# Optimization experiments

Hardware: AMD Instinct MI355X
Metric: run time of the kernel (lower is better)

## Reference

```python
import jax, jax.numpy as jnp
import numpy as np

IN_DIM, OUT_DIM = 128, 128
NUM, K = 5, 3            # knot intervals, spline order
SIZE = IN_DIM * OUT_DIM
BATCH = 512
NOISE = 0.1


def extend_knots_uniform(grid, k):
    # grid: (s, n_knots). Uniformly extend by k knots on each side.
    if k <= 0:
        return grid
    step = (grid[:, -1:] - grid[:, :1]) / (grid.shape[1] - 1)  # (s,1)
    left = grid[:, :1] - step * jnp.arange(k, 0, -1, dtype=grid.dtype)[None, :]
    right = grid[:, -1:] + step * jnp.arange(1, k + 1, dtype=grid.dtype)[None, :]
    return jnp.concatenate([left, grid, right], axis=1)


def cox_deboor(x, t, k):
    # x: (s, n), t: (s, m) extended knots -> B: (s, m-1-k, n)
    xt = x[:, None, :]                                   # (s,1,n)
    B = ((xt >= t[:, :-1, None]) & (xt < t[:, 1:, None])).astype(x.dtype)  # (s, m-1, n)
    m = t.shape[1]
    for r in range(1, k + 1):
        denom_a = jnp.maximum(t[:, r:m - 1] - t[:, :m - 1 - r], 1e-14)
        alpha = (xt - t[:, :m - 1 - r, None]) / denom_a[:, :, None]
        denom_b = jnp.maximum(t[:, r + 1:m] - t[:, 1:m - r], 1e-14)
        beta = (t[:, r + 1:m, None] - xt) / denom_b[:, :, None]
        B = alpha * B[:, :-1, :] + beta * B[:, 1:, :]    # (s, m-1-r, n)
    return B


def setup_inputs() -> dict:
    key = jax.random.key(0)
    kx, kc = jax.random.split(key)
    x = jax.random.normal(kx, (BATCH, IN_DIM), dtype=jnp.float32)
    knots = jnp.linspace(-1.0, 1.0, NUM + 1, dtype=jnp.float32)
    grid = jnp.tile(knots[None, :], (SIZE, 1))                       # (size, num+1)
    coef = jax.random.normal(kc, (SIZE, NUM + K), dtype=jnp.float32) * NOISE
    scale_base = jnp.ones((SIZE,), dtype=jnp.float32)
    scale_sp = jnp.ones((SIZE,), dtype=jnp.float32)
    mask = jnp.ones((SIZE,), dtype=jnp.float32)
    return {"x": x, "grid": grid, "coef": coef,
            "scale_base": scale_base, "scale_sp": scale_sp, "mask": mask}


def reference(x, grid, coef, scale_base, scale_sp, mask):
    batch = x.shape[0]
    # einsum('ij,k->ikj').reshape(b, size).T : row o*in_dim+i holds x[:, i]
    x_exp = jnp.tile(x, (1, OUT_DIM)).T                  # (size, batch)
    base_act = jax.nn.silu(x_exp)
    t_ext = extend_knots_uniform(grid, K)                # (size, num+1+2k)
    B = cox_deboor(x_exp, t_ext, K)                      # (size, num+k, batch)
    spline_val = jnp.einsum('sbn,sb->sn', B, coef)       # (size, batch)
    out = (scale_base[:, None] * base_act + scale_sp[:, None] * spline_val) * mask[:, None]
    out3 = out.reshape(OUT_DIM, IN_DIM, batch)           # permute(2,0,1).sum(dim=2)
    return out3.sum(axis=1).T                            # (batch, out_dim)
```

## Files before the change

### kernel.cpp

```cpp
#include <hip/hip_runtime.h>
#include <math.h>

constexpr int IN_DIM  = 128;
constexpr int OUT_DIM = 128;
constexpr int BATCH   = 512;
constexpr int TN  = 8;
constexpr int TO  = 32;
constexpr int IC  = 16;
constexpr int NC  = IN_DIM / IC;
constexpr int TOP = TO + 1;

__global__ __launch_bounds__(256, 1) void kan_fused(
    const float* __restrict__ x,
    const float* __restrict__ grid,
    const float* __restrict__ coef,
    const float* __restrict__ scale_base,
    const float* __restrict__ scale_sp,
    const float* __restrict__ mask,
    float* __restrict__ out)
{
    __shared__ float4 Ps[TN * IN_DIM * 2];
    __shared__ float  Pb[IN_DIM * TN];
    __shared__ float4 Cs0[IC * TOP];
    __shared__ float4 Cs1[IC * TOP];
    __shared__ float  Vb [IC * TOP];

    const int t  = threadIdx.x;
    const int b  = blockIdx.x;
    const int o0 = (b & 3) * TO;
    const int n0 = (b >> 2) * TN;

    const float g0 = grid[0];
    const float g5 = grid[5];
    const float h  = (g5 - g0) * 0.2f;
    float tk[12];
    tk[0] = g0 - 3.f * h; tk[1] = g0 - 2.f * h; tk[2] = g0 - h;
    tk[3] = grid[0]; tk[4] = grid[1]; tk[5] = grid[2];
    tk[6] = grid[3]; tk[7] = grid[4]; tk[8] = grid[5];
    tk[9] = g5 + h; tk[10] = g5 + 2.f * h; tk[11] = g5 + 3.f * h;
    const float inv1 = 1.0f / h;
    const float invr[3] = {inv1, inv1 * 0.5f, inv1 * (1.0f / 3.0f)};

    #pragma unroll
    for (int r = 0; r < 4; r++) {
        const int v = r * 256 + t;
        const int n = v >> 7;
        const int i = v & 127;
        const float xv = x[(n0 + n) * IN_DIM + i];
        float B[11];
        #pragma unroll
        for (int j = 0; j < 11; j++)
            B[j] = (xv >= tk[j] && xv < tk[j + 1]) ? 1.0f : 0.0f;
        #pragma unroll
        for (int rr = 1; rr <= 3; rr++) {
            const float iv = invr[rr - 1];
            #pragma unroll
            for (int j = 0; j + rr < 11; j++)
                B[j] = (xv - tk[j]) * iv * B[j] + (tk[j + rr + 1] - xv) * iv * B[j + 1];
        }
        Ps[(n * IN_DIM + i) * 2 + 0] = make_float4(B[0], B[1], B[2], B[3]);
        Ps[(n * IN_DIM + i) * 2 + 1] = make_float4(B[4], B[5], B[6], B[7]);
        Pb[i * TN + n] = xv / (1.0f + __expf(-xv));
    }

    float4 rc[4];
    float  rv[2];

#define LOADREG(cc)                                                          \
    {                                                                        \
        _Pragma("unroll")                                                    \
        for (int r = 0; r < 4; r++) {                                        \
            const int fi = r * 256 + t;                                      \
            const int oo = fi >> 5;                    \
            const int w  = fi & 31;                \
            const int s  = (o0 + oo) * IN_DIM + (cc) * IC + (w >> 1);        \
            float4 cv = ((const float4*)coef)[(size_t)s * 2 + (w & 1)];      \
            const float vv = scale_sp[s] * mask[s];                          \
            cv.x *= vv; cv.y *= vv; cv.z *= vv; cv.w *= vv;                  \
            rc[r] = cv;                                                      \
        }                                                                    \
        _Pragma("unroll")                                                    \
        for (int r = 0; r < 2; r++) {                                        \
            const int v  = r * 256 + t;                                      \
            const int oo = v >> 4;                    \
            const int s  = (o0 + oo) * IN_DIM + (cc) * IC + (v & 15);        \
            rv[r] = scale_base[s] * mask[s];                                 \
        }                                                                    \
    }

#define WRITELDS()                                                           \
    {                                                                        \
        _Pragma("unroll")                                                    \
        for (int r = 0; r < 4; r++) {                                        \
            const int fi = r * 256 + t;                                      \
            const int oo = fi >> 5;                                          \
            const int w  = fi & 31;                                          \
            const int i  = w >> 1;                                           \
            if (w & 1) Cs1[i * TOP + oo] = rc[r];                            \
            else       Cs0[i * TOP + oo] = rc[r];                            \
        }                                                                    \
        _Pragma("unroll")                                                    \
        for (int r = 0; r < 2; r++) {                                        \
            const int v = r * 256 + t;                                       \
            Vb[(v & 15) * TOP + (v >> 4)] = rv[r];                           \
        }                                                                    \
    }

    LOADREG(0);
    WRITELDS();
    __syncthreads();

    const int o = t & 31;
    const int n = t >> 5;
    const float4* __restrict__ psn = &Ps[n * IN_DIM * 2];
    const float*  __restrict__ pbn = &Pb[n];

    float acc = 0.f;
    #pragma unroll 1
    for (int c = 0; c < NC; c++) {
        if (c + 1 < NC) LOADREG(c + 1);
        #pragma unroll
        for (int il = 0; il < IC; il++) {
            const int i = c * IC + il;
            const float4 c0 = Cs0[il * TOP + o];
            const float4 c1 = Cs1[il * TOP + o];
            const float4 a0 = psn[2 * i];
            const float4 a1 = psn[2 * i + 1];
            const float vb  = Vb[il * TOP + o];
            const float pb  = pbn[i * TN];
            acc += c0.x * a0.x + c0.y * a0.y + c0.z * a0.z + c0.w * a0.w
                 + c1.x * a1.x + c1.y * a1.y + c1.z * a1.z + c1.w * a1.w
                 + vb * pb;
        }
        if (c + 1 < NC) {
            __syncthreads();
            WRITELDS();
            __syncthreads();
        }
    }

    out[(size_t)(n0 + n) * OUT_DIM + o0 + o] = acc;
#undef LOADREG
#undef WRITELDS
}

extern "C" void kernel_launch(void* const* d_in, const int* in_sizes, int n_in,
                              void* d_out, int out_size, void* d_ws, size_t ws_size,
                              hipStream_t stream) {
    (void)in_sizes; (void)n_in; (void)out_size; (void)d_ws; (void)ws_size;
    const float* x          = (const float*)d_in[0];
    const float* grid       = (const float*)d_in[1];
    const float* coef       = (const float*)d_in[2];
    const float* scale_base = (const float*)d_in[3];
    const float* scale_sp   = (const float*)d_in[4];
    const float* mask       = (const float*)d_in[5];

    kan_fused<<<dim3(256), dim3(256), 0, stream>>>(
        x, grid, coef, scale_base, scale_sp, mask, (float*)d_out);
}
```

Baseline: 79.80 us.

## Split input dim across thread groups and read coefficients directly from global

```diff
diff --git a/kernel.cpp b/kernel.cpp
--- a/kernel.cpp
+++ b/kernel.cpp
@@ -5,12 +5,13 @@
 constexpr int OUT_DIM = 128;
 constexpr int BATCH   = 512;
 constexpr int TN  = 8;
-constexpr int TO  = 32;
-constexpr int IC  = 16;
-constexpr int NC  = IN_DIM / IC;
-constexpr int TOP = TO + 1;
+constexpr int TO  = 16;
+constexpr int IG  = 4;
+constexpr int IPT = IN_DIM / IG;
+constexpr int PSR = 2 * IN_DIM + 1;
+constexpr int SR  = IN_DIM + 4;
 
-__global__ __launch_bounds__(256, 1) void kan_fused(
+__global__ __launch_bounds__(512, 4) void kan_fused(
     const float* __restrict__ x,
     const float* __restrict__ grid,
     const float* __restrict__ coef,
@@ -19,16 +20,16 @@
     const float* __restrict__ mask,
     float* __restrict__ out)
 {
-    __shared__ float4 Ps[TN * IN_DIM * 2];
-    __shared__ float  Pb[IN_DIM * TN];
-    __shared__ float4 Cs0[IC * TOP];
-    __shared__ float4 Cs1[IC * TOP];
-    __shared__ float  Vb [IC * TOP];
+    __shared__ float4 Ps[TN * PSR];
+    __shared__ float  Pb[TN * SR];
+    __shared__ float  Sm[TO * SR];
+    __shared__ float  Vb[TO * SR];
+    __shared__ float  Red[IG * TN * TO];
 
     const int t  = threadIdx.x;
     const int b  = blockIdx.x;
-    const int o0 = (b & 3) * TO;
-    const int n0 = (b >> 2) * TN;
+    const int o0 = (b & 7) * TO;
+    const int n0 = (b >> 3) * TN;
 
     const float g0 = grid[0];
     const float g5 = grid[5];
@@ -42,8 +43,8 @@
     const float invr[3] = {inv1, inv1 * 0.5f, inv1 * (1.0f / 3.0f)};
 
     #pragma unroll
-    for (int r = 0; r < 4; r++) {
-        const int v = r * 256 + t;
+    for (int r = 0; r < 2; r++) {
+        const int v = r * 512 + t;
         const int n = v >> 7;
         const int i = v & 127;
         const float xv = x[(n0 + n) * IN_DIM + i];
@@ -58,90 +59,69 @@
             for (int j = 0; j + rr < 11; j++)
                 B[j] = (xv - tk[j]) * iv * B[j] + (tk[j + rr + 1] - xv) * iv * B[j + 1];
         }
-        Ps[(n * IN_DIM + i) * 2 + 0] = make_float4(B[0], B[1], B[2], B[3]);
-        Ps[(n * IN_DIM + i) * 2 + 1] = make_float4(B[4], B[5], B[6], B[7]);
-        Pb[i * TN + n] = xv / (1.0f + __expf(-xv));
+        Ps[n * PSR + 2 * i + 0] = make_float4(B[0], B[1], B[2], B[3]);
+        Ps[n * PSR + 2 * i + 1] = make_float4(B[4], B[5], B[6], B[7]);
+        Pb[n * SR + i] = xv / (1.0f + __expf(-xv));
     }
 
-    float4 rc[4];
-    float  rv[2];
-
-#define LOADREG(cc)                                                          \
-    {                                                                        \
-        _Pragma("unroll")                                                    \
-        for (int r = 0; r < 4; r++) {                                        \
-            const int fi = r * 256 + t;                                      \
-            const int oo = fi >> 5;                    \
-            const int w  = fi & 31;                \
-            const int s  = (o0 + oo) * IN_DIM + (cc) * IC + (w >> 1);        \
-            float4 cv = ((const float4*)coef)[(size_t)s * 2 + (w & 1)];      \
-            const float vv = scale_sp[s] * mask[s];                          \
-            cv.x *= vv; cv.y *= vv; cv.z *= vv; cv.w *= vv;                  \
-            rc[r] = cv;                                                      \
-        }                                                                    \
-        _Pragma("unroll")                                                    \
-        for (int r = 0; r < 2; r++) {                                        \
-            const int v  = r * 256 + t;                                      \
-            const int oo = v >> 4;                    \
-            const int s  = (o0 + oo) * IN_DIM + (cc) * IC + (v & 15);        \
-            rv[r] = scale_base[s] * mask[s];                                 \
-        }                                                                    \
+    #pragma unroll
+    for (int r = 0; r < 4; r++) {
+        const int v = r * 512 + t;
+        const int o = v >> 7;
+        const int i = v & 127;
+        const int s = (o0 + o) * IN_DIM + i;
+        const float mv = mask[s];
+        Sm[o * SR + i] = scale_sp[s]   * mv;
+        Vb[o * SR + i] = scale_base[s] * mv;
     }
-
-#define WRITELDS()                                                           \
-    {                                                                        \
-        _Pragma("unroll")                                                    \
-        for (int r = 0; r < 4; r++) {                                        \
-            const int fi = r * 256 + t;                                      \
-            const int oo = fi >> 5;                                          \
-            const int w  = fi & 31;                                          \
-            const int i  = w >> 1;                                           \
-            if (w & 1) Cs1[i * TOP + oo] = rc[r];                            \
-            else       Cs0[i * TOP + oo] = rc[r];                            \
-        }                                                                    \
-        _Pragma("unroll")                                                    \
-        for (int r = 0; r < 2; r++) {                                        \
-            const int v = r * 256 + t;                                       \
-            Vb[(v & 15) * TOP + (v >> 4)] = rv[r];                           \
-        }                                                                    \
-    }
-
-    LOADREG(0);
-    WRITELDS();
     __syncthreads();
 
-    const int o = t & 31;
-    const int n = t >> 5;
-    const float4* __restrict__ psn = &Ps[n * IN_DIM * 2];
-    const float*  __restrict__ pbn = &Pb[n];
+    const int o  = t & 15;
+    const int n  = (t >> 4) & 7;
+    const int ig = t >> 7;
+    const float4* __restrict__ cf  = (const float4*)coef;
+    const float4* __restrict__ psn = &Ps[n * PSR];
+    const float*  __restrict__ pbn = &Pb[n * SR];
+    const float*  __restrict__ smo = &Sm[o * SR];
+    const float*  __restrict__ vbo = &Vb[o * SR];
+    const size_t  crow = (size_t)(o0 + o) * IN_DIM;
+    const int     ibase = ig * IPT;
 
     float acc = 0.f;
     #pragma unroll 1
-    for (int c = 0; c < NC; c++) {
-        if (c + 1 < NC) LOADREG(c + 1);
+    for (int g = 0; g < IPT / 8; g++) {
+        const int i8 = ibase + g * 8;
+        const float4 sm0 = *(const float4*)&smo[i8];
+        const float4 sm1 = *(const float4*)&smo[i8 + 4];
+        const float4 vb0 = *(const float4*)&vbo[i8];
+        const float4 vb1 = *(const float4*)&vbo[i8 + 4];
+        const float4 pb0 = *(const float4*)&pbn[i8];
+        const float4 pb1 = *(const float4*)&pbn[i8 + 4];
+        const float sm_[8] = {sm0.x, sm0.y, sm0.z, sm0.w, sm1.x, sm1.y, sm1.z, sm1.w};
+        const float vb_[8] = {vb0.x, vb0.y, vb0.z, vb0.w, vb1.x, vb1.y, vb1.z, vb1.w};
+        const float pb_[8] = {pb0.x, pb0.y, pb0.z, pb0.w, pb1.x, pb1.y, pb1.z, pb1.w};
         #pragma unroll
-        for (int il = 0; il < IC; il++) {
-            const int i = c * IC + il;
-            const float4 c0 = Cs0[il * TOP + o];
-            const float4 c1 = Cs1[il * TOP + o];
+        for (int il = 0; il < 8; il++) {
+            const int i = i8 + il;
+            const float4 c0 = cf[(crow + i) * 2 + 0];
+            const float4 c1 = cf[(crow + i) * 2 + 1];
             const float4 a0 = psn[2 * i];
             const float4 a1 = psn[2 * i + 1];
-            const float vb  = Vb[il * TOP + o];
-            const float pb  = pbn[i * TN];
-            acc += c0.x * a0.x + c0.y * a0.y + c0.z * a0.z + c0.w * a0.w
-                 + c1.x * a1.x + c1.y * a1.y + c1.z * a1.z + c1.w * a1.w
-                 + vb * pb;
-        }
-        if (c + 1 < NC) {
-            __syncthreads();
-            WRITELDS();
-            __syncthreads();
+            const float w = c0.x * a0.x + c0.y * a0.y + c0.z * a0.z + c0.w * a0.w
+                          + c1.x * a1.x + c1.y * a1.y + c1.z * a1.z + c1.w * a1.w;
+            acc = fmaf(sm_[il], w, acc);
+            acc = fmaf(vb_[il], pb_[il], acc);
         }
     }
 
-    out[(size_t)(n0 + n) * OUT_DIM + o0 + o] = acc;
-#undef LOADREG
-#undef WRITELDS
+    Red[ig * (TN * TO) + (n * TO + o)] = acc;
+    __syncthreads();
+    if (t < TN * TO) {
+        const float s = Red[t] + Red[128 + t] + Red[256 + t] + Red[384 + t];
+        const int n2 = t >> 4;
+        const int o2 = t & 15;
+        out[(size_t)(n0 + n2) * OUT_DIM + o0 + o2] = s;
+    }
 }
 
 extern "C" void kernel_launch(void* const* d_in, const int* in_sizes, int n_in,
@@ -155,6 +135,6 @@
     const float* scale_sp   = (const float*)d_in[4];
     const float* mask       = (const float*)d_in[5];
 
-    kan_fused<<<dim3(256), dim3(256), 0, stream>>>(
+    kan_fused<<<dim3(512), dim3(512), 0, stream>>>(
         x, grid, coef, scale_base, scale_sp, mask, (float*)d_out);
 }
```

New measurement: 94.79 us. 18.8% more time.
